# Kernel optimization log

Hardware: AMD Instinct MI355X
Metric: run time of the kernel (lower is better)

The kernel has to match this reference:

```python
import jax, jax.numpy as jnp
import numpy as np

DIM = 1024
HEADS = 16
DIM_HEAD = 64
INNER = HEADS * DIM_HEAD  # 1024
EPS = 1e-5


def layer_norm(x, g, b):
    mu = jnp.mean(x, axis=-1, keepdims=True)
    var = jnp.var(x, axis=-1, keepdims=True)
    return (x - mu) * jax.lax.rsqrt(var + EPS) * g + b


def setup_inputs() -> dict:
    key = jax.random.key(0)
    ks = jax.random.split(key, 8)
    s = 0.02
    return {
        "x": jax.random.normal(ks[0], (2, 2048, DIM), dtype=jnp.float32),
        "w_qkv": jax.random.normal(ks[1], (DIM, 3 * INNER), dtype=jnp.float32) * s,
        "w_out": jax.random.normal(ks[2], (INNER, DIM), dtype=jnp.float32) * s,
        "b_out": jnp.zeros((DIM,), jnp.float32),
        "g1": jnp.ones((DIM,), jnp.float32),
        "bt1": jnp.zeros((DIM,), jnp.float32),
        "g2": jnp.ones((DIM,), jnp.float32),
        "bt2": jnp.zeros((DIM,), jnp.float32),
        "w1": jax.random.normal(ks[3], (DIM, DIM), dtype=jnp.float32) * s,  # ff hidden = dim_out = DIM
        "b1": jnp.zeros((DIM,), jnp.float32),
        "w2": jax.random.normal(ks[4], (DIM, DIM), dtype=jnp.float32) * s,
        "b2": jnp.zeros((DIM,), jnp.float32),
    }


def reference(x, w_qkv, w_out, b_out, g1, bt1, g2, bt2, w1, b1, w2, b2):
    b, n, _ = x.shape
    scale = DIM_HEAD ** (-0.5)
    x_in = x
    xl = layer_norm(x, g1, bt1)
    qkv = xl @ w_qkv  # [b, n, 3*inner]
    q, k, v = jnp.split(qkv, 3, axis=-1)
    def split_heads(t):
        return t.reshape(b, n, HEADS, DIM_HEAD).transpose(0, 2, 1, 3)  # b h n d
    q, k, v = map(split_heads, (q, k, v))
    dots = jnp.einsum('bhid,bhjd->bhij', q, k) * scale
    attn = jax.nn.softmax(dots, axis=-1)
    out = jnp.einsum('bhij,bhjd->bhid', attn, v)
    out = out.transpose(0, 2, 1, 3).reshape(b, n, INNER)
    out = out @ w_out + b_out
    out = out + x_in
    h = layer_norm(out, g2, bt2)
    h = jax.nn.gelu(h @ w1 + b1, approximate=False) @ w2 + b2
    return h + out
```

## Files before the change

kernel.cpp:

```cpp
#include <hip/hip_runtime.h>
#include <math.h>

typedef __attribute__((ext_vector_type(4))) float f32x4;
typedef __attribute__((ext_vector_type(8))) short bf16x8;
typedef __attribute__((ext_vector_type(8))) unsigned short u16x8;

#define DIM 1024
#define SEQ 2048
#define NHEADS 16
#define DH 64

__device__ __forceinline__ unsigned short f2bf(float f) {
    unsigned int u = __builtin_bit_cast(unsigned int, f);
    u += 0x7fffu + ((u >> 16) & 1u);
    return (unsigned short)(u >> 16);
}

__device__ __forceinline__ unsigned int cvt_pk_bf16(float lo, float hi) {
    unsigned int r;
    asm("v_cvt_pk_bf16_f32 %0, %1, %2" : "=v"(r) : "v"(lo), "v"(hi));
    return r;
}

__device__ __forceinline__ float fexp2(float x) {
    float r;
    asm("v_exp_f32 %0, %1" : "=v"(r) : "v"(x));
    return r;
}

__device__ __forceinline__ void gld16(const unsigned short* g, unsigned short* l) {
    __builtin_amdgcn_global_load_lds((const __attribute__((address_space(1))) void*)g,
                                     (__attribute__((address_space(3))) void*)l, 16, 0, 0);
}

__global__ __launch_bounds__(256) void wtrans_all(const float* __restrict__ wq,
                                                  const float* __restrict__ wo,
                                                  const float* __restrict__ wf1,
                                                  const float* __restrict__ wf2,
                                                  unsigned short* __restrict__ oq,
                                                  unsigned short* __restrict__ oo,
                                                  unsigned short* __restrict__ of1,
                                                  unsigned short* __restrict__ of2, float sc) {
    int z = blockIdx.z;
    int bxi = blockIdx.x;
    if (z > 0 && bxi >= 32) return;
    const float* w = z == 0 ? wq : z == 1 ? wo : z == 2 ? wf1 : wf2;
    unsigned short* wt = z == 0 ? oq : z == 1 ? oo : z == 2 ? of1 : of2;
    int N = z == 0 ? 3072 : 1024;
    int scale_n = z == 0 ? 1024 : 0;
    const int K = 1024;
    __shared__ float t[32][33];
    int tid = threadIdx.x;
    int n0 = bxi * 32, k0 = blockIdx.y * 32;
    int c = tid & 31, rb = tid >> 5;
#pragma unroll
    for (int i = 0; i < 4; ++i) {
        int r = rb + i * 8;
        t[r][c] = w[(size_t)(k0 + r) * N + n0 + c];
    }
    __syncthreads();
#pragma unroll
    for (int i = 0; i < 4; ++i) {
        int r = rb + i * 8;
        float v = t[c][r];
        if (n0 + r < scale_n) v *= sc;
        wt[(size_t)(n0 + r) * K + k0 + c] = f2bf(v);
    }
}

__global__ __launch_bounds__(256) void ln_kernel(const float* __restrict__ x,
                                                 const float* __restrict__ g,
                                                 const float* __restrict__ bt,
                                                 unsigned short* __restrict__ o) {
    int row = blockIdx.x, tid = threadIdx.x;
    const float4* xr = (const float4*)(x + (size_t)row * DIM);
    float4 v = xr[tid];
    float s1 = v.x + v.y + v.z + v.w;
    float s2 = v.x * v.x + v.y * v.y + v.z * v.z + v.w * v.w;
#pragma unroll
    for (int m = 32; m >= 1; m >>= 1) {
        s1 += __shfl_xor(s1, m);
        s2 += __shfl_xor(s2, m);
    }
    __shared__ float r1[4], r2[4];
    int w = tid >> 6;
    if ((tid & 63) == 0) { r1[w] = s1; r2[w] = s2; }
    __syncthreads();
    s1 = r1[0] + r1[1] + r1[2] + r1[3];
    s2 = r2[0] + r2[1] + r2[2] + r2[3];
    float mu = s1 * (1.0f / DIM);
    float var = s2 * (1.0f / DIM) - mu * mu;
    float rstd = rsqrtf(var + 1e-5f);
    float4 g4 = ((const float4*)g)[tid];
    float4 b4 = ((const float4*)bt)[tid];
    ushort4 ov;
    ov.x = f2bf((v.x - mu) * rstd * g4.x + b4.x);
    ov.y = f2bf((v.y - mu) * rstd * g4.y + b4.y);
    ov.z = f2bf((v.z - mu) * rstd * g4.z + b4.z);
    ov.w = f2bf((v.w - mu) * rstd * g4.w + b4.w);
    *(ushort4*)(o + (size_t)row * DIM + tid * 4) = ov;
}

template <int BN, int BK, int OBF, int BIAS, int GELU_, int RESID>
__global__ __launch_bounds__(256) void gemm_kernel(const unsigned short* __restrict__ A,
                                                   const unsigned short* __restrict__ BT,
                                                   void* __restrict__ C,
                                                   const float* __restrict__ bias,
                                                   const float* __restrict__ resid,
                                                   int M, int N, int K, int nbx) {
    constexpr int U = BK / 8;
    constexpr int NAU = 128 * U;
    constexpr int NBU = BN * U;
    constexpr int PT = (NAU + NBU) / 256;
    constexpr int NJ = BN / 32;
    constexpr int KK = BK / 32;
    __shared__ unsigned short As[3][128 * BK];
    __shared__ unsigned short Bs[3][BN * BK];
    int tid = threadIdx.x;
    int lane = tid & 63, w = tid >> 6;
    int l15 = lane & 15, lhi = lane >> 4;
    int nwg = gridDim.x, wg = blockIdx.x;
    int swz = (wg & 7) * (nwg >> 3) + (wg >> 3);
    int bx = swz % nbx, by = swz / nbx;
    int row0 = by * 128, col0 = bx * BN;
    int wrow = (w >> 1) * 64, wcol = (w & 1) * (16 * NJ);
    f32x4 zero = {0.f, 0.f, 0.f, 0.f};
    f32x4 acc[4][NJ];
#pragma unroll
    for (int i = 0; i < 4; ++i)
#pragma unroll
        for (int j = 0; j < NJ; ++j) acc[i][j] = zero;
    auto stage = [&](int buf, int kt) {
#pragma unroll
        for (int p = 0; p < PT; ++p) {
            if (p * 256 < NAU) {
                int u = tid + p * 256;
                int r = u / U, cu = u % U;
                int scu = cu ^ (r & (U - 1));
                gld16(A + (size_t)(row0 + r) * K + kt * BK + scu * 8, &As[buf][0] + u * 8);
            } else {
                int ub = tid + p * 256 - NAU;
                int r = ub / U, cu = ub % U;
                int scu = cu ^ (r & (U - 1));
                gld16(BT + (size_t)(col0 + r) * K + kt * BK + scu * 8, &Bs[buf][0] + ub * 8);
            }
        }
    };
    int nk = K / BK;
    stage(0, 0);
    stage(1, 1);
    asm volatile("s_waitcnt vmcnt(%0)" ::"i"(PT) : "memory");
    __builtin_amdgcn_s_barrier();
    __builtin_amdgcn_sched_barrier(0);
    int cur = 0;
    for (int kt = 0; kt < nk; ++kt) {
        int nxt2 = cur + 2 >= 3 ? cur - 1 : cur + 2;
        if (kt + 2 < nk) stage(nxt2, kt + 2);
        const unsigned short* Ab = &As[cur][0];
        const unsigned short* Bb = &Bs[cur][0];
        bf16x8 af[4][KK], bfr[NJ][KK];
#pragma unroll
        for (int i = 0; i < 4; ++i)
#pragma unroll
            for (int kk = 0; kk < KK; ++kk) {
                int rr = wrow + i * 16 + l15;
                int up = (kk * 4 + lhi) ^ (rr & (U - 1));
                af[i][kk] = *(const bf16x8*)&Ab[rr * BK + up * 8];
            }
#pragma unroll
        for (int j = 0; j < NJ; ++j)
#pragma unroll
            for (int kk = 0; kk < KK; ++kk) {
                int rr = wcol + j * 16 + l15;
                int up = (kk * 4 + lhi) ^ (rr & (U - 1));
                bfr[j][kk] = *(const bf16x8*)&Bb[rr * BK + up * 8];
            }
#pragma unroll
        for (int kk = 0; kk < KK; ++kk)
#pragma unroll
            for (int i = 0; i < 4; ++i)
#pragma unroll
                for (int j = 0; j < NJ; ++j)
                    acc[i][j] = __builtin_amdgcn_mfma_f32_16x16x32_bf16(af[i][kk], bfr[j][kk],
                                                                        acc[i][j], 0, 0, 0);
        __builtin_amdgcn_sched_barrier(0);
        if (kt + 1 < nk) {
            if (kt + 2 < nk)
                asm volatile("s_waitcnt vmcnt(%0)" ::"i"(PT) : "memory");
            else
                asm volatile("s_waitcnt vmcnt(0)" ::: "memory");
            __builtin_amdgcn_s_barrier();
            __builtin_amdgcn_sched_barrier(0);
        }
        cur = cur + 1 == 3 ? 0 : cur + 1;
    }
#pragma unroll
    for (int i = 0; i < 4; ++i)
#pragma unroll
        for (int j = 0; j < NJ; ++j)
#pragma unroll
            for (int r = 0; r < 4; ++r) {
                int row = row0 + wrow + i * 16 + lhi * 4 + r;
                int col = col0 + wcol + j * 16 + l15;
                float v = acc[i][j][r];
                if (BIAS) v += bias[col];
                if (GELU_) v = 0.5f * v * (1.0f + erff(v * 0.70710678118f));
                if (RESID) v += resid[(size_t)row * N + col];
                if (OBF)
                    ((unsigned short*)C)[(size_t)row * N + col] = f2bf(v);
                else
                    ((float*)C)[(size_t)row * N + col] = v;
            }
}

__global__ __launch_bounds__(256) void vtrans_kernel(const unsigned short* __restrict__ qkv,
                                                     unsigned short* __restrict__ vt) {
    __shared__ unsigned short t[64 * 72];
    int tid = threadIdx.x;
    int nt = blockIdx.x & 31, h = (blockIdx.x >> 5) & 15, b = blockIdx.x >> 9;
#pragma unroll
    for (int p = 0; p < 2; ++p) {
        int c = tid + p * 256;
        int n = c >> 3, s = (c & 7) * 8;
        *(uint4*)&t[n * 72 + s] =
            *(const uint4*)(qkv + (size_t)(b * SEQ + nt * 64 + n) * 3072 + 2048 + h * 64 + s);
    }
    __syncthreads();
#pragma unroll
    for (int p = 0; p < 2; ++p) {
        int c = tid + p * 256;
        int d = c >> 3, s0 = (c & 7) * 8;
        u16x8 val;
#pragma unroll
        for (int j = 0; j < 8; ++j) {
            int s = s0 + j;
            int sig = (s & 32) | ((s & 4) << 2) | ((s & 24) >> 1) | (s & 3);
            val[j] = t[sig * 72 + d];
        }
        *(u16x8*)(vt + ((size_t)(b * NHEADS + h) * DH + d) * SEQ + nt * 64 + s0) = val;
    }
}

__global__ __launch_bounds__(256, 1) void attn_kernel(const unsigned short* __restrict__ qkv,
                                                      const unsigned short* __restrict__ vt,
                                                      unsigned short* __restrict__ o) {
    __shared__ unsigned short Ks[3][64 * 64];
    __shared__ unsigned short Vs[3][64 * 64];
    int tid = threadIdx.x;
    int lane = tid & 63, w = tid >> 6;
    int l15 = lane & 15, lhi = lane >> 4;
    int wg = blockIdx.x;
    int swz = (wg & 7) * 32 + (wg >> 3);
    int qt = swz & 7, h = (swz >> 3) & 15, b = swz >> 7;
    bf16x8 qf[4][2];
#pragma unroll
    for (int qg = 0; qg < 4; ++qg) {
        const unsigned short* qb =
            qkv + (size_t)(b * SEQ + qt * 256 + w * 64 + qg * 16 + l15) * 3072 + h * DH;
        qf[qg][0] = *(const bf16x8*)(qb + lhi * 8);
        qf[qg][1] = *(const bf16x8*)(qb + 32 + lhi * 8);
    }
    f32x4 zero = {0.f, 0.f, 0.f, 0.f};
    f32x4 oacc[4][4], lacc[4];
#pragma unroll
    for (int qg = 0; qg < 4; ++qg) {
        lacc[qg] = zero;
#pragma unroll
        for (int i = 0; i < 4; ++i) oacc[qg][i] = zero;
    }
    const short one_s = (short)0x3F80;
    bf16x8 ones = {one_s, one_s, one_s, one_s, one_s, one_s, one_s, one_s};
    int srow = tid >> 3;
    int scx = (tid & 7) ^ (srow & 7);
    const unsigned short* kb = qkv + (size_t)b * SEQ * 3072 + 1024 + h * DH;
    const unsigned short* vb = vt + (size_t)(b * NHEADS + h) * DH * SEQ;
    const unsigned short* k0 = kb + (size_t)srow * 3072 + scx * 8;
    const unsigned short* v0 = vb + (size_t)srow * SEQ + scx * 8;
    auto stage = [&](int buf, int kt) {
        unsigned short* lk = &Ks[buf][0] + tid * 8;
        unsigned short* lv = &Vs[buf][0] + tid * 8;
        gld16(k0 + (size_t)kt * 64 * 3072, lk);
        gld16(k0 + ((size_t)kt * 64 + 32) * 3072, lk + 2048);
        gld16(v0 + kt * 64, lv);
        gld16(v0 + (size_t)32 * SEQ + kt * 64, lv + 2048);
    };
    const int NT = SEQ / 64;
    stage(0, 0);
    stage(1, 1);
    asm volatile("s_waitcnt vmcnt(4)" ::: "memory");
    __builtin_amdgcn_s_barrier();
    __builtin_amdgcn_sched_barrier(0);
    int kx = l15 & 7;
    int cur = 0;
    for (int kt = 0; kt < NT; ++kt) {
        int nxt2 = cur + 2 >= 3 ? cur - 1 : cur + 2;
        if (kt + 2 < NT) stage(nxt2, kt + 2);
        const unsigned short* Kc = &Ks[cur][0];
        const unsigned short* Vc = &Vs[cur][0];
        bf16x8 kf0[4], kf1[4];
#pragma unroll
        for (int nt = 0; nt < 4; ++nt) {
            kf0[nt] = *(const bf16x8*)&Kc[(nt * 16 + l15) * 64 + ((lhi ^ kx) * 8)];
            kf1[nt] = *(const bf16x8*)&Kc[(nt * 16 + l15) * 64 + (((4 + lhi) ^ kx) * 8)];
        }
        bf16x8 pf[4][2];
#pragma unroll
        for (int qg = 0; qg < 4; ++qg) {
            f32x4 sacc[4];
#pragma unroll
            for (int nt = 0; nt < 4; ++nt) {
                f32x4 z = __builtin_amdgcn_mfma_f32_16x16x32_bf16(kf0[nt], qf[qg][0], zero, 0, 0, 0);
                sacc[nt] = __builtin_amdgcn_mfma_f32_16x16x32_bf16(kf1[nt], qf[qg][1], z, 0, 0, 0);
            }
#pragma unroll
            for (int kc = 0; kc < 2; ++kc) {
                union { bf16x8 v; unsigned int u[4]; } pu;
                pu.u[0] = cvt_pk_bf16(fexp2(sacc[2 * kc][0]), fexp2(sacc[2 * kc][1]));
                pu.u[1] = cvt_pk_bf16(fexp2(sacc[2 * kc][2]), fexp2(sacc[2 * kc][3]));
                pu.u[2] = cvt_pk_bf16(fexp2(sacc[2 * kc + 1][0]), fexp2(sacc[2 * kc + 1][1]));
                pu.u[3] = cvt_pk_bf16(fexp2(sacc[2 * kc + 1][2]), fexp2(sacc[2 * kc + 1][3]));
                pf[qg][kc] = pu.v;
            }
        }
#pragma unroll
        for (int dt = 0; dt < 4; ++dt)
#pragma unroll
            for (int kc = 0; kc < 2; ++kc) {
                bf16x8 vf = *(const bf16x8*)&Vc[(dt * 16 + l15) * 64 + (((kc * 4 + lhi) ^ kx) * 8)];
#pragma unroll
                for (int qg = 0; qg < 4; ++qg)
                    oacc[qg][dt] =
                        __builtin_amdgcn_mfma_f32_16x16x32_bf16(vf, pf[qg][kc], oacc[qg][dt], 0, 0, 0);
            }
#pragma unroll
        for (int qg = 0; qg < 4; ++qg) {
            lacc[qg] = __builtin_amdgcn_mfma_f32_16x16x32_bf16(ones, pf[qg][0], lacc[qg], 0, 0, 0);
            lacc[qg] = __builtin_amdgcn_mfma_f32_16x16x32_bf16(ones, pf[qg][1], lacc[qg], 0, 0, 0);
        }
        __builtin_amdgcn_sched_barrier(0);
        if (kt + 1 < NT) {
            if (kt + 2 < NT)
                asm volatile("s_waitcnt vmcnt(4)" ::: "memory");
            else
                asm volatile("s_waitcnt vmcnt(0)" ::: "memory");
            __builtin_amdgcn_s_barrier();
            __builtin_amdgcn_sched_barrier(0);
        }
        cur = cur + 1 == 3 ? 0 : cur + 1;
    }
#pragma unroll
    for (int qg = 0; qg < 4; ++qg) {
        float rl = 1.0f / lacc[qg][0];
        size_t orow = (size_t)(b * SEQ + qt * 256 + w * 64 + qg * 16 + l15) * DIM + h * DH;
#pragma unroll
        for (int dt = 0; dt < 4; ++dt) {
            ushort4 st;
            st.x = f2bf(oacc[qg][dt][0] * rl);
            st.y = f2bf(oacc[qg][dt][1] * rl);
            st.z = f2bf(oacc[qg][dt][2] * rl);
            st.w = f2bf(oacc[qg][dt][3] * rl);
            *(ushort4*)(o + orow + dt * 16 + lhi * 4) = st;
        }
    }
}

extern "C" void kernel_launch(void* const* d_in, const int* in_sizes, int n_in,
                              void* d_out, int out_size, void* d_ws, size_t ws_size,
                              hipStream_t stream) {
    (void)in_sizes; (void)n_in; (void)out_size; (void)ws_size;
    const float* x = (const float*)d_in[0];
    const float* w_qkv = (const float*)d_in[1];
    const float* w_out = (const float*)d_in[2];
    const float* b_out = (const float*)d_in[3];
    const float* g1 = (const float*)d_in[4];
    const float* bt1 = (const float*)d_in[5];
    const float* g2 = (const float*)d_in[6];
    const float* bt2 = (const float*)d_in[7];
    const float* w1 = (const float*)d_in[8];
    const float* b1 = (const float*)d_in[9];
    const float* w2 = (const float*)d_in[10];
    const float* b2 = (const float*)d_in[11];
    float* out = (float*)d_out;

    char* ws = (char*)d_ws;
    size_t off = 0;
    auto alloc = [&](size_t bytes) {
        void* p = ws + off;
        off += (bytes + 255) & ~(size_t)255;
        return p;
    };
    const int R = 2 * SEQ;
    unsigned short* xl    = (unsigned short*)alloc((size_t)R * DIM * 2);
    unsigned short* wqkvT = (unsigned short*)alloc((size_t)3 * DIM * DIM * 2);
    unsigned short* woutT = (unsigned short*)alloc((size_t)DIM * DIM * 2);
    unsigned short* w1T   = (unsigned short*)alloc((size_t)DIM * DIM * 2);
    unsigned short* w2T   = (unsigned short*)alloc((size_t)DIM * DIM * 2);
    unsigned short* qkvb  = (unsigned short*)alloc((size_t)R * 3 * DIM * 2);
    unsigned short* vtb   = (unsigned short*)alloc((size_t)R * DIM * 2);
    unsigned short* attO  = (unsigned short*)alloc((size_t)R * DIM * 2);
    unsigned short* h2    = (unsigned short*)alloc((size_t)R * DIM * 2);
    unsigned short* ffn1  = (unsigned short*)alloc((size_t)R * DIM * 2);

    const float CS = 0.125f * 1.44269504f;
    wtrans_all<<<dim3(96, 32, 4), 256, 0, stream>>>(w_qkv, w_out, w1, w2, wqkvT, woutT, w1T, w2T, CS);

    ln_kernel<<<R, 256, 0, stream>>>(x, g1, bt1, xl);
    gemm_kernel<128, 32, 1, 0, 0, 0><<<dim3((3 * DIM / 128) * (R / 128)), 256, 0, stream>>>(
        xl, wqkvT, qkvb, nullptr, nullptr, R, 3 * DIM, DIM, 3 * DIM / 128);
    vtrans_kernel<<<2 * NHEADS * (SEQ / 64), 256, 0, stream>>>(qkvb, vtb);
    attn_kernel<<<2 * NHEADS * (SEQ / 256), 256, 0, stream>>>(qkvb, vtb, attO);
    gemm_kernel<64, 64, 0, 1, 0, 1><<<dim3((DIM / 64) * (R / 128)), 256, 0, stream>>>(
        attO, woutT, out, b_out, x, R, DIM, DIM, DIM / 64);
    ln_kernel<<<R, 256, 0, stream>>>(out, g2, bt2, h2);
    gemm_kernel<64, 64, 1, 1, 1, 0><<<dim3((DIM / 64) * (R / 128)), 256, 0, stream>>>(
        h2, w1T, ffn1, b1, nullptr, R, DIM, DIM, DIM / 64);
    gemm_kernel<64, 64, 0, 1, 0, 1><<<dim3((DIM / 64) * (R / 128)), 256, 0, stream>>>(
        ffn1, w2T, out, b2, out, R, DIM, DIM, DIM / 64);
}
```

Baseline: 176.0 us.

## Shrink attention query tile to 64 rows and use double-buffered K/V

Each attention workgroup now handles 64 query rows (16 per wave) instead of 256, so the grid is four times larger (1024 blocks versus 256). The K/V LDS ring drops from triple to double buffering, and the launch-bounds occupancy hint of 1 is removed. This should cut per-thread register use and raise occupancy and parallelism across the CUs. In exchange, each K/V tile loaded into LDS now feeds four times fewer queries, multiplying global and LDS traffic, and the prefetch depth is shallower, with a full vmcnt(0) wait every iteration.

```diff
diff --git a/kernel.cpp b/kernel.cpp
--- a/kernel.cpp
+++ b/kernel.cpp
@@ -241,33 +241,25 @@
     }
 }
 
-__global__ __launch_bounds__(256, 1) void attn_kernel(const unsigned short* __restrict__ qkv,
-                                                      const unsigned short* __restrict__ vt,
-                                                      unsigned short* __restrict__ o) {
-    __shared__ unsigned short Ks[3][64 * 64];
-    __shared__ unsigned short Vs[3][64 * 64];
+__global__ __launch_bounds__(256) void attn_kernel(const unsigned short* __restrict__ qkv,
+                                                   const unsigned short* __restrict__ vt,
+                                                   unsigned short* __restrict__ o) {
+    __shared__ unsigned short Ks[2][64 * 64];
+    __shared__ unsigned short Vs[2][64 * 64];
     int tid = threadIdx.x;
     int lane = tid & 63, w = tid >> 6;
     int l15 = lane & 15, lhi = lane >> 4;
     int wg = blockIdx.x;
-    int swz = (wg & 7) * 32 + (wg >> 3);
-    int qt = swz & 7, h = (swz >> 3) & 15, b = swz >> 7;
-    bf16x8 qf[4][2];
-#pragma unroll
-    for (int qg = 0; qg < 4; ++qg) {
-        const unsigned short* qb =
-            qkv + (size_t)(b * SEQ + qt * 256 + w * 64 + qg * 16 + l15) * 3072 + h * DH;
-        qf[qg][0] = *(const bf16x8*)(qb + lhi * 8);
-        qf[qg][1] = *(const bf16x8*)(qb + 32 + lhi * 8);
-    }
+    int swz = (wg & 7) * 128 + (wg >> 3);
+    int qt = swz & 31, h = (swz >> 5) & 15, b = swz >> 9;
+    const unsigned short* qb =
+        qkv + (size_t)(b * SEQ + qt * 64 + w * 16 + l15) * 3072 + h * DH;
+    bf16x8 qf0 = *(const bf16x8*)(qb + lhi * 8);
+    bf16x8 qf1 = *(const bf16x8*)(qb + 32 + lhi * 8);
     f32x4 zero = {0.f, 0.f, 0.f, 0.f};
-    f32x4 oacc[4][4], lacc[4];
-#pragma unroll
-    for (int qg = 0; qg < 4; ++qg) {
-        lacc[qg] = zero;
-#pragma unroll
-        for (int i = 0; i < 4; ++i) oacc[qg][i] = zero;
-    }
+    f32x4 oacc[4], lacc = zero;
+#pragma unroll
+    for (int i = 0; i < 4; ++i) oacc[i] = zero;
     const short one_s = (short)0x3F80;
     bf16x8 ones = {one_s, one_s, one_s, one_s, one_s, one_s, one_s, one_s};
     int srow = tid >> 3;
@@ -286,81 +278,59 @@
     };
     const int NT = SEQ / 64;
     stage(0, 0);
-    stage(1, 1);
-    asm volatile("s_waitcnt vmcnt(4)" ::: "memory");
+    asm volatile("s_waitcnt vmcnt(0)" ::: "memory");
     __builtin_amdgcn_s_barrier();
     __builtin_amdgcn_sched_barrier(0);
     int kx = l15 & 7;
-    int cur = 0;
     for (int kt = 0; kt < NT; ++kt) {
-        int nxt2 = cur + 2 >= 3 ? cur - 1 : cur + 2;
-        if (kt + 2 < NT) stage(nxt2, kt + 2);
+        int cur = kt & 1;
+        if (kt + 1 < NT) stage(cur ^ 1, kt + 1);
         const unsigned short* Kc = &Ks[cur][0];
         const unsigned short* Vc = &Vs[cur][0];
-        bf16x8 kf0[4], kf1[4];
+        f32x4 sacc[4];
 #pragma unroll
         for (int nt = 0; nt < 4; ++nt) {
-            kf0[nt] = *(const bf16x8*)&Kc[(nt * 16 + l15) * 64 + ((lhi ^ kx) * 8)];
-            kf1[nt] = *(const bf16x8*)&Kc[(nt * 16 + l15) * 64 + (((4 + lhi) ^ kx) * 8)];
-        }
-        bf16x8 pf[4][2];
-#pragma unroll
-        for (int qg = 0; qg < 4; ++qg) {
-            f32x4 sacc[4];
-#pragma unroll
-            for (int nt = 0; nt < 4; ++nt) {
-                f32x4 z = __builtin_amdgcn_mfma_f32_16x16x32_bf16(kf0[nt], qf[qg][0], zero, 0, 0, 0);
-                sacc[nt] = __builtin_amdgcn_mfma_f32_16x16x32_bf16(kf1[nt], qf[qg][1], z, 0, 0, 0);
-            }
-#pragma unroll
-            for (int kc = 0; kc < 2; ++kc) {
-                union { bf16x8 v; unsigned int u[4]; } pu;
-                pu.u[0] = cvt_pk_bf16(fexp2(sacc[2 * kc][0]), fexp2(sacc[2 * kc][1]));
-                pu.u[1] = cvt_pk_bf16(fexp2(sacc[2 * kc][2]), fexp2(sacc[2 * kc][3]));
-                pu.u[2] = cvt_pk_bf16(fexp2(sacc[2 * kc + 1][0]), fexp2(sacc[2 * kc + 1][1]));
-                pu.u[3] = cvt_pk_bf16(fexp2(sacc[2 * kc + 1][2]), fexp2(sacc[2 * kc + 1][3]));
-                pf[qg][kc] = pu.v;
-            }
+            bf16x8 kf0 = *(const bf16x8*)&Kc[(nt * 16 + l15) * 64 + ((lhi ^ kx) * 8)];
+            bf16x8 kf1 = *(const bf16x8*)&Kc[(nt * 16 + l15) * 64 + (((4 + lhi) ^ kx) * 8)];
+            f32x4 z = __builtin_amdgcn_mfma_f32_16x16x32_bf16(kf0, qf0, zero, 0, 0, 0);
+            sacc[nt] = __builtin_amdgcn_mfma_f32_16x16x32_bf16(kf1, qf1, z, 0, 0, 0);
+        }
+        bf16x8 pf[2];
+#pragma unroll
+        for (int kc = 0; kc < 2; ++kc) {
+            union { bf16x8 v; unsigned int u[4]; } pu;
+            pu.u[0] = cvt_pk_bf16(fexp2(sacc[2 * kc][0]), fexp2(sacc[2 * kc][1]));
+            pu.u[1] = cvt_pk_bf16(fexp2(sacc[2 * kc][2]), fexp2(sacc[2 * kc][3]));
+            pu.u[2] = cvt_pk_bf16(fexp2(sacc[2 * kc + 1][0]), fexp2(sacc[2 * kc + 1][1]));
+            pu.u[3] = cvt_pk_bf16(fexp2(sacc[2 * kc + 1][2]), fexp2(sacc[2 * kc + 1][3]));
+            pf[kc] = pu.v;
         }
 #pragma unroll
         for (int dt = 0; dt < 4; ++dt)
 #pragma unroll
             for (int kc = 0; kc < 2; ++kc) {
                 bf16x8 vf = *(const bf16x8*)&Vc[(dt * 16 + l15) * 64 + (((kc * 4 + lhi) ^ kx) * 8)];
-#pragma unroll
-                for (int qg = 0; qg < 4; ++qg)
-                    oacc[qg][dt] =
-                        __builtin_amdgcn_mfma_f32_16x16x32_bf16(vf, pf[qg][kc], oacc[qg][dt], 0, 0, 0);
-            }
-#pragma unroll
-        for (int qg = 0; qg < 4; ++qg) {
-            lacc[qg] = __builtin_amdgcn_mfma_f32_16x16x32_bf16(ones, pf[qg][0], lacc[qg], 0, 0, 0);
-            lacc[qg] = __builtin_amdgcn_mfma_f32_16x16x32_bf16(ones, pf[qg][1], lacc[qg], 0, 0, 0);
-        }
+                oacc[dt] = __builtin_amdgcn_mfma_f32_16x16x32_bf16(vf, pf[kc], oacc[dt], 0, 0, 0);
+            }
+        lacc = __builtin_amdgcn_mfma_f32_16x16x32_bf16(ones, pf[0], lacc, 0, 0, 0);
+        lacc = __builtin_amdgcn_mfma_f32_16x16x32_bf16(ones, pf[1], lacc, 0, 0, 0);
         __builtin_amdgcn_sched_barrier(0);
         if (kt + 1 < NT) {
-            if (kt + 2 < NT)
-                asm volatile("s_waitcnt vmcnt(4)" ::: "memory");
-            else
-                asm volatile("s_waitcnt vmcnt(0)" ::: "memory");
+            asm volatile("s_waitcnt vmcnt(0)" ::: "memory");
             __builtin_amdgcn_s_barrier();
             __builtin_amdgcn_sched_barrier(0);
         }
-        cur = cur + 1 == 3 ? 0 : cur + 1;
-    }
-#pragma unroll
-    for (int qg = 0; qg < 4; ++qg) {
-        float rl = 1.0f / lacc[qg][0];
-        size_t orow = (size_t)(b * SEQ + qt * 256 + w * 64 + qg * 16 + l15) * DIM + h * DH;
-#pragma unroll
-        for (int dt = 0; dt < 4; ++dt) {
-            ushort4 st;
-            st.x = f2bf(oacc[qg][dt][0] * rl);
-            st.y = f2bf(oacc[qg][dt][1] * rl);
-            st.z = f2bf(oacc[qg][dt][2] * rl);
-            st.w = f2bf(oacc[qg][dt][3] * rl);
-            *(ushort4*)(o + orow + dt * 16 + lhi * 4) = st;
-        }
+    }
+    float rl = 1.0f / lacc[0];
+    size_t orow = (size_t)(b * SEQ + qt * 64 + w * 16 + l15) * DIM + h * DH;
+#pragma unroll
+    for (int dt = 0; dt < 4; ++dt) {
+        ushort4 st;
+        st.x = f2bf(oacc[dt][0] * rl);
+        st.y = f2bf(oacc[dt][1] * rl);
+        st.z = f2bf(oacc[dt][2] * rl);
+        st.w = f2bf(oacc[dt][3] * rl);
+        *(ushort4*)(o + orow + dt * 16 + lhi * 4) = st;
     }
 }
 
@@ -408,7 +378,7 @@
     gemm_kernel<128, 32, 1, 0, 0, 0><<<dim3((3 * DIM / 128) * (R / 128)), 256, 0, stream>>>(
         xl, wqkvT, qkvb, nullptr, nullptr, R, 3 * DIM, DIM, 3 * DIM / 128);
     vtrans_kernel<<<2 * NHEADS * (SEQ / 64), 256, 0, stream>>>(qkvb, vtb);
-    attn_kernel<<<2 * NHEADS * (SEQ / 256), 256, 0, stream>>>(qkvb, vtb, attO);
+    attn_kernel<<<2 * NHEADS * (SEQ / 64), 256, 0, stream>>>(qkvb, vtb, attO);
     gemm_kernel<64, 64, 0, 1, 0, 1><<<dim3((DIM / 64) * (R / 128)), 256, 0, stream>>>(
         attO, woutT, out, b_out, x, R, DIM, DIM, DIM / 64);
     ln_kernel<<<R, 256, 0, stream>>>(out, g2, bt2, h2);
```

Measured after the change: 168.4 us. 1.05x faster.
